# Kernel tuning notes

Measured on AMD Instinct MI355X. Metric: run time of the kernel, lower is better.

The kernel has to match this reference:

```python
import jax, jax.numpy as jnp
import numpy as np

N_NODES = 100000


def _graph_conv(x, W, b, src, dst, inv_sqrt_out, inv_sqrt_in):
    # DGL GraphConv, norm='both':  D_in^{-1/2} A D_out^{-1/2} X W + b
    h = x * inv_sqrt_out[:, None]
    if W.shape[0] > W.shape[1]:
        # in_feats > out_feats: transform first (cheaper aggregation)
        h = h @ W
        m = jax.ops.segment_sum(h[src], dst, num_segments=N_NODES)
    else:
        m = jax.ops.segment_sum(h[src], dst, num_segments=N_NODES)
        m = m @ W
    return m * inv_sqrt_in[:, None] + b


def _degree_norms(src, dst):
    ones = jnp.ones(src.shape[0], dtype=jnp.float32)
    out_deg = jax.ops.segment_sum(ones, src, num_segments=N_NODES)
    in_deg = jax.ops.segment_sum(ones, dst, num_segments=N_NODES)
    # DGL clamps degree to min 1 (allow_zero_in_degree)
    return jnp.clip(out_deg, 1.0) ** -0.5, jnp.clip(in_deg, 1.0) ** -0.5


def setup_inputs() -> dict:
    key = jax.random.key(0)
    ks = jax.random.split(key, 8)
    E = 800000
    in_feats, h1, h2, nc = 128, 256, 128, 40
    return {
        "features": jax.random.normal(ks[0], (N_NODES, in_feats), dtype=jnp.float32),
        "src": jax.random.randint(ks[1], (E,), 0, N_NODES),
        "dst": jax.random.randint(ks[2], (E,), 0, N_NODES),
        "W1": jax.random.normal(ks[3], (in_feats, h1), dtype=jnp.float32) * (2.0 / (in_feats + h1)) ** 0.5,
        "b1": jnp.zeros((h1,), dtype=jnp.float32),
        "W2": jax.random.normal(ks[4], (h1, h2), dtype=jnp.float32) * (2.0 / (h1 + h2)) ** 0.5,
        "b2": jnp.zeros((h2,), dtype=jnp.float32),
        "W3": jax.random.normal(ks[5], (h2, nc), dtype=jnp.float32) * (2.0 / (h2 + nc)) ** 0.5,
        "b3": jnp.zeros((nc,), dtype=jnp.float32),
    }


def reference(features, src, dst, W1, b1, W2, b2, W3, b3):
    inv_out, inv_in = _degree_norms(src, dst)
    h = _graph_conv(features, W1, b1, src, dst, inv_out, inv_in)
    h = jax.nn.relu(h)
    h = _graph_conv(h, W2, b2, src, dst, inv_out, inv_in)
    h = jax.nn.relu(h)
    return _graph_conv(h, W3, b3, src, dst, inv_out, inv_in)
```

## Files before the change

kernel.cpp:

```cpp
#include <hip/hip_runtime.h>

#define N_NODES 100000
#define SCAN_NB 128
#define SCAN_TPB 256
#define NREP 8

typedef _Float16 half_t;
typedef __attribute__((ext_vector_type(8))) _Float16 v8h;
typedef __attribute__((ext_vector_type(4))) _Float16 v4h;
typedef __attribute__((ext_vector_type(4))) float v4f;


__global__ void prep1(const int* __restrict__ src, const int* __restrict__ dst,
                      int* __restrict__ ocntR, int* __restrict__ icntR,
                      int* __restrict__ loc, int E,
                      const float* __restrict__ W1, const float* __restrict__ W2,
                      const float* __restrict__ W3, half_t* __restrict__ Wt1,
                      half_t* __restrict__ Wt2, half_t* __restrict__ Wt3) {
    int t = blockIdx.x * blockDim.x + threadIdx.x;
    if (t < E) {
        int r = (t >> 6) & (NREP - 1);
        loc[t] = atomicAdd(&icntR[r * N_NODES + dst[t]], 1);
        atomicAdd(&ocntR[r * N_NODES + src[t]], 1);
    } else {
        int u = t - E;
        if (u < 32768) {
            int n = u >> 7, k = u & 127;
            Wt1[u] = (half_t)W1[(size_t)k * 256 + n];
        } else if (u < 65536) {
            int w = u - 32768;
            int n = w >> 8, k = w & 255;
            Wt2[w] = (half_t)W2[(size_t)k * 128 + n];
        } else if (u < 70656) {
            int w = u - 65536;
            int n = w >> 7, k = w & 127;
            Wt3[w] = (half_t)W3[(size_t)k * 40 + n];
        }
    }
}


__global__ __launch_bounds__(SCAN_TPB) void scan_reduce(const int* __restrict__ icntR,
                                                        int* __restrict__ blockSum, int n) {
    __shared__ int s[SCAN_TPB];
    int chunk = (n + SCAN_NB - 1) / SCAN_NB;
    int beg = blockIdx.x * chunk;
    int end = min(beg + chunk, n);
    int sum = 0;
    for (int i = beg + threadIdx.x; i < end; i += SCAN_TPB) {
#pragma unroll
        for (int r = 0; r < NREP; ++r) sum += icntR[r * N_NODES + i];
    }
    s[threadIdx.x] = sum;
    __syncthreads();
    for (int off = SCAN_TPB / 2; off > 0; off >>= 1) {
        if (threadIdx.x < off) s[threadIdx.x] += s[threadIdx.x + off];
        __syncthreads();
    }
    if (threadIdx.x == 0) blockSum[blockIdx.x] = s[0];
}

__global__ __launch_bounds__(SCAN_NB) void scan_offsets(int* __restrict__ blockSum,
                                                        int* __restrict__ rowptr_total) {
    __shared__ int s[SCAN_NB];
    int tid = threadIdx.x;
    int v = blockSum[tid];
    s[tid] = v;
    __syncthreads();
    for (int off = 1; off < SCAN_NB; off <<= 1) {
        int t = (tid >= off) ? s[tid - off] : 0;
        __syncthreads();
        s[tid] += t;
        __syncthreads();
    }
    blockSum[tid] = s[tid] - v;
    if (tid == SCAN_NB - 1) rowptr_total[0] = s[tid];
}

__global__ __launch_bounds__(SCAN_TPB) void scan_final(int* __restrict__ icntR,
                                                       const int* __restrict__ ocntR,
                                                       const int* __restrict__ blockSum,
                                                       int* __restrict__ rowptr,
                                                       float* __restrict__ invIn,
                                                       float* __restrict__ invOut, int n) {
    __shared__ int s[SCAN_TPB];
    int chunk = (n + SCAN_NB - 1) / SCAN_NB;
    int beg = blockIdx.x * chunk;
    int end = min(beg + chunk, n);
    int carry = blockSum[blockIdx.x];
    for (int base = beg; base < end; base += SCAN_TPB) {
        int i = base + threadIdx.x;
        int v = 0;
        if (i < end) {
            int run = 0;
#pragma unroll
            for (int r = 0; r < NREP; ++r) {
                int c = icntR[r * N_NODES + i];
                icntR[r * N_NODES + i] = run;
                run += c;
            }
            v = run;
        }
        s[threadIdx.x] = v;
        __syncthreads();
        for (int off = 1; off < SCAN_TPB; off <<= 1) {
            int t = (threadIdx.x >= off) ? s[threadIdx.x - off] : 0;
            __syncthreads();
            s[threadIdx.x] += t;
            __syncthreads();
        }
        int excl = s[threadIdx.x] - v;
        if (i < end) {
            rowptr[i] = carry + excl;
            int o = 0;
#pragma unroll
            for (int r = 0; r < NREP; ++r) o += ocntR[r * N_NODES + i];
            invOut[i] = rsqrtf((float)max(o, 1));
            invIn[i] = rsqrtf((float)max(v, 1));
        }
        int roundSum = s[SCAN_TPB - 1];
        __syncthreads();
        carry += roundSum;
    }
}


__global__ void prep2(const int* __restrict__ src, const int* __restrict__ dst,
                      const int* __restrict__ loc, const int* __restrict__ icntR,
                      const int* __restrict__ rowptr,
                      int* __restrict__ eidx, int E,
                      const float* __restrict__ x, const float* __restrict__ invOut,
                      half_t* __restrict__ xh) {
    int t = blockIdx.x * blockDim.x + threadIdx.x;
    if (t < E) {
        int d = dst[t];
        int r = (t >> 6) & (NREP - 1);
        eidx[rowptr[d] + icntR[r * N_NODES + d] + loc[t]] = src[t];
    } else {
        int u = t - E;
        if (u < N_NODES * 32) {
            int n = u >> 5;
            float4 v = ((const float4*)x)[u];
            float s = invOut[n];
            v4h h;
            h[0] = (half_t)(v.x * s);
            h[1] = (half_t)(v.y * s);
            h[2] = (half_t)(v.z * s);
            h[3] = (half_t)(v.w * s);
            *(v4h*)(xh + (size_t)u * 4) = h;
        }
    }
}


template <int F>
__device__ __forceinline__ void gather_row(const half_t* __restrict__ x,
                                           const int* __restrict__ eidx,
                                           int beg, int end, int c, float* acc) {
    const half_t* __restrict__ xc = x + (size_t)c * 8;
    int n = end - beg;
    int nb = n & ~3;
    int j = 0;
    if (nb) {
        int i0 = eidx[beg + 0], i1 = eidx[beg + 1], i2 = eidx[beg + 2], i3 = eidx[beg + 3];
        do {
            v8h v0 = *(const v8h*)(xc + (size_t)i0 * F);
            v8h v1 = *(const v8h*)(xc + (size_t)i1 * F);
            v8h v2 = *(const v8h*)(xc + (size_t)i2 * F);
            v8h v3 = *(const v8h*)(xc + (size_t)i3 * F);
            j += 4;
            if (j < nb) {
                i0 = eidx[beg + j + 0];
                i1 = eidx[beg + j + 1];
                i2 = eidx[beg + j + 2];
                i3 = eidx[beg + j + 3];
            }
#pragma unroll
            for (int q = 0; q < 8; ++q)
                acc[q] += ((float)v0[q] + (float)v1[q]) + ((float)v2[q] + (float)v3[q]);
        } while (j < nb);
    }
    for (; j < n; ++j) {
        int s = eidx[beg + j];
        v8h val = *(const v8h*)(xc + (size_t)s * F);
#pragma unroll
        for (int q = 0; q < 8; ++q) acc[q] += (float)val[q];
    }
}


__global__ __launch_bounds__(256, 8) void gather1(
    const half_t* __restrict__ xh, const int* __restrict__ rowptr,
    const int* __restrict__ eidx, half_t* __restrict__ A1) {
    int t = blockIdx.x * 256 + threadIdx.x;
    int n = t >> 4, c = t & 15;
    if (n >= N_NODES) return;
    float acc[8] = {};
    gather_row<128>(xh, eidx, rowptr[n], rowptr[n + 1], c, acc);
    v8h o;
#pragma unroll
    for (int q = 0; q < 8; ++q) o[q] = (half_t)acc[q];
    *(v8h*)(A1 + (size_t)n * 128 + c * 8) = o;
}

__global__ __launch_bounds__(256, 8) void gather2(
    const half_t* __restrict__ t2, const int* __restrict__ rowptr,
    const int* __restrict__ eidx, const float* __restrict__ invIn,
    const float* __restrict__ invOut, const float* __restrict__ b2,
    half_t* __restrict__ A2) {
    int t = blockIdx.x * 256 + threadIdx.x;
    int n = t >> 4, c = t & 15;
    if (n >= N_NODES) return;
    float acc[8] = {};
    gather_row<128>(t2, eidx, rowptr[n], rowptr[n + 1], c, acc);
    float ii = invIn[n], io = invOut[n];
    float4 blo = ((const float4*)b2)[c * 2];
    float4 bhi = ((const float4*)b2)[c * 2 + 1];
    float bb[8] = {blo.x, blo.y, blo.z, blo.w, bhi.x, bhi.y, bhi.z, bhi.w};
    v8h o;
#pragma unroll
    for (int q = 0; q < 8; ++q)
        o[q] = (half_t)fmaxf((acc[q] * ii + bb[q]) * io, 0.f);
    *(v8h*)(A2 + (size_t)n * 128 + c * 8) = o;
}


__global__ __launch_bounds__(512) void mlp12(
    const half_t* __restrict__ A1, const half_t* __restrict__ Wt1,
    const half_t* __restrict__ Wt2,
    const float* __restrict__ invIn, const float* __restrict__ invOut,
    const float* __restrict__ b1, half_t* __restrict__ t2) {
    constexpr int K1 = 128, K2 = 256, N2 = 128;
    constexpr int LDA = K1 + 8;
    constexpr int LDH = K2 + 8;
    __shared__ half_t As[64][LDA];
    __shared__ half_t h1S[64][LDH];
    __shared__ float iiS[64], ioS[64];
    const int tid = threadIdx.x;
    const int wave = tid >> 6, lane = tid & 63;
    const int quad = lane >> 4, l16 = lane & 15;
    const int m0 = blockIdx.x * 64;
    const int n0 = wave * 32;

    v8h b[2][4];
    float bv[2];
#pragma unroll
    for (int j = 0; j < 2; ++j) {
        int gn = n0 + j * 16 + l16;
        bv[j] = b1[gn];
#pragma unroll
        for (int kc = 0; kc < 4; ++kc)
            b[j][kc] = *(const v8h*)(Wt1 + (size_t)gn * K1 + kc * 32 + quad * 8);
    }
    if (tid < 64) {
        int gm = m0 + tid;
        bool ok = gm < N_NODES;
        iiS[tid] = ok ? invIn[gm] : 0.f;
        ioS[tid] = ok ? invOut[gm] : 0.f;
    }

#pragma unroll
    for (int p = 0; p < 2; ++p) {
        int task = tid + p * 512;
        int r = task >> 4, c = task & 15;
        int gm = m0 + r;
        v8h v = (gm < N_NODES) ? *(const v8h*)(A1 + (size_t)gm * K1 + c * 8)
                               : (v8h)(half_t)0;
        *(v8h*)&As[r][c * 8] = v;
    }
    __syncthreads();

    for (int mt = 0; mt < 4; ++mt) {
        v8h a[4];
#pragma unroll
        for (int kc = 0; kc < 4; ++kc)
            a[kc] = *(const v8h*)&As[mt * 16 + l16][kc * 32 + quad * 8];
        v4f acc[2] = {};
#pragma unroll
        for (int kc = 0; kc < 4; ++kc)
#pragma unroll
            for (int j = 0; j < 2; ++j)
                acc[j] = __builtin_amdgcn_mfma_f32_16x16x32_f16(a[kc], b[j][kc], acc[j], 0, 0, 0);
#pragma unroll
        for (int j = 0; j < 2; ++j) {
            int cn = n0 + j * 16 + l16;
#pragma unroll
            for (int r = 0; r < 4; ++r) {
                int lr = mt * 16 + quad * 4 + r;
                float z = (acc[j][r] * iiS[lr] + bv[j]) * ioS[lr];
                h1S[lr][cn] = (half_t)fmaxf(z, 0.f);
            }
        }
    }

    v8h b2[8];
    const int n02 = wave * 16;
    {
        int gn = n02 + l16;
#pragma unroll
        for (int kc = 0; kc < 8; ++kc)
            b2[kc] = *(const v8h*)(Wt2 + (size_t)gn * K2 + kc * 32 + quad * 8);
    }
    __syncthreads();

    for (int mt = 0; mt < 4; ++mt) {
        v8h a2[8];
#pragma unroll
        for (int kc = 0; kc < 8; ++kc)
            a2[kc] = *(const v8h*)&h1S[mt * 16 + l16][kc * 32 + quad * 8];
        v4f acc2 = {};
#pragma unroll
        for (int kc = 0; kc < 8; ++kc)
            acc2 = __builtin_amdgcn_mfma_f32_16x16x32_f16(a2[kc], b2[kc], acc2, 0, 0, 0);
        int gn = n02 + l16;
#pragma unroll
        for (int r = 0; r < 4; ++r) {
            int gm = m0 + mt * 16 + quad * 4 + r;
            if (gm < N_NODES) t2[(size_t)gm * N2 + gn] = (half_t)acc2[r];
        }
    }
}


__global__ __launch_bounds__(256) void mlp3(
    const half_t* __restrict__ A2, const half_t* __restrict__ Wt3,
    half_t* __restrict__ t3) {
    constexpr int K = 128, N = 40, LDA = K + 8;
    __shared__ half_t As[64][LDA];
    const int tid = threadIdx.x;
    const int wave = tid >> 6, lane = tid & 63;
    const int quad = lane >> 4, l16 = lane & 15;
    const int m0 = blockIdx.x * 64;

    v8h b[3][4];
#pragma unroll
    for (int j = 0; j < 3; ++j) {
        int gn = j * 16 + l16;
#pragma unroll
        for (int kc = 0; kc < 4; ++kc)
            b[j][kc] = (gn < N) ? *(const v8h*)(Wt3 + (size_t)gn * K + kc * 32 + quad * 8)
                                : (v8h)(half_t)0;
    }

#pragma unroll
    for (int p = 0; p < 4; ++p) {
        int task = tid + p * 256;
        int r = task >> 4, c = task & 15;
        int gm = m0 + r;
        v8h v = (gm < N_NODES) ? *(const v8h*)(A2 + (size_t)gm * K + c * 8)
                               : (v8h)(half_t)0;
        *(v8h*)&As[r][c * 8] = v;
    }
    __syncthreads();

    {
        int mt = wave;
        v8h a[4];
#pragma unroll
        for (int kc = 0; kc < 4; ++kc)
            a[kc] = *(const v8h*)&As[mt * 16 + l16][kc * 32 + quad * 8];
        v4f acc[3] = {};
#pragma unroll
        for (int kc = 0; kc < 4; ++kc)
#pragma unroll
            for (int j = 0; j < 3; ++j)
                acc[j] = __builtin_amdgcn_mfma_f32_16x16x32_f16(a[kc], b[j][kc], acc[j], 0, 0, 0);
#pragma unroll
        for (int j = 0; j < 3; ++j) {
            int gn = j * 16 + l16;
            if (gn >= N) continue;
#pragma unroll
            for (int r = 0; r < 4; ++r) {
                int gm = m0 + mt * 16 + quad * 4 + r;
                if (gm < N_NODES) t3[(size_t)gm * N + gn] = (half_t)acc[j][r];
            }
        }
    }
}


__global__ __launch_bounds__(256, 8) void gather_final(
    const half_t* __restrict__ x,
    const int* __restrict__ rowptr, const int* __restrict__ eidx,
    float* __restrict__ out, const float* __restrict__ invIn,
    const float* __restrict__ bias) {
    constexpr int F = 40, V = 5;
    int t = blockIdx.x * blockDim.x + threadIdx.x;
    int n = t / V;
    int v = t - n * V;
    if (n >= N_NODES) return;
    float acc[8] = {};
    gather_row<F>(x, eidx, rowptr[n], rowptr[n + 1], v, acc);
    float ii = invIn[n];
    float* o = out + (size_t)n * F + v * 8;
#pragma unroll
    for (int q = 0; q < 8; ++q) o[q] = acc[q] * ii + bias[v * 8 + q];
}


extern "C" void kernel_launch(void* const* d_in, const int* in_sizes, int n_in,
                              void* d_out, int out_size, void* d_ws, size_t ws_size,
                              hipStream_t stream) {
    const float* x  = (const float*)d_in[0];
    const int* src  = (const int*)d_in[1];
    const int* dst  = (const int*)d_in[2];
    const float* W1 = (const float*)d_in[3];
    const float* b1 = (const float*)d_in[4];
    const float* W2 = (const float*)d_in[5];
    const float* b2 = (const float*)d_in[6];
    const float* W3 = (const float*)d_in[7];
    const float* b3 = (const float*)d_in[8];
    float* out = (float*)d_out;
    const int E = in_sizes[1];

    char* ws = (char*)d_ws;
    float* inv_out = (float*)ws;
    float* inv_in  = (float*)(ws + 400000);
    int* rowptr    = (int*)(ws + 800000);
    int* eidx      = (int*)(ws + 1600256);
    int* blockSum  = (int*)(ws + 4800256);
    half_t* Wt1    = (half_t*)(ws + 4800768);
    half_t* Wt2    = (half_t*)(ws + 4866304);
    half_t* Wt3    = (half_t*)(ws + 4931840);
    half_t* bufA   = (half_t*)(ws + 5000192);
    half_t* bufB   = (half_t*)(ws + 30600192);
    int* loc   = (int*)bufB;
    int* icntR = (int*)((char*)bufB + (((size_t)E * 4 + 255) & ~(size_t)255));
    int* ocntR = icntR + NREP * N_NODES;

    hipMemsetAsync(icntR, 0, (size_t)NREP * N_NODES * 4 * 2, stream);
    prep1<<<(E + 70656 + 255) / 256, 256, 0, stream>>>(src, dst, ocntR, icntR, loc, E,
                                                       W1, W2, W3, Wt1, Wt2, Wt3);
    scan_reduce<<<SCAN_NB, SCAN_TPB, 0, stream>>>(icntR, blockSum, N_NODES);
    scan_offsets<<<1, SCAN_NB, 0, stream>>>(blockSum, rowptr + N_NODES);
    scan_final<<<SCAN_NB, SCAN_TPB, 0, stream>>>(icntR, ocntR, blockSum, rowptr,
                                                 inv_in, inv_out, N_NODES);
    prep2<<<(E + N_NODES * 32 + 255) / 256, 256, 0, stream>>>(src, dst, loc, icntR, rowptr,
                                                              eidx, E, x, inv_out, bufA);

    const int NBG = (N_NODES * 16 + 255) / 256;
    const int NB  = (N_NODES + 63) / 64;

    gather1<<<NBG, 256, 0, stream>>>(bufA, rowptr, eidx, bufB);
    mlp12<<<NB, 512, 0, stream>>>(bufB, Wt1, Wt2, inv_in, inv_out, b1, bufA);
    gather2<<<NBG, 256, 0, stream>>>(bufA, rowptr, eidx, inv_in, inv_out, b2, bufB);
    mlp3<<<NB, 256, 0, stream>>>(bufB, Wt3, bufA);
    gather_final<<<(N_NODES * 5 + 255) / 256, 256, 0, stream>>>(
        bufA, rowptr, eidx, out, inv_in, b3);
}
```

Before: 338.8 us.

## Replace global atomic degree counting with LDS-privatized sliced histograms

Degree counting now runs in shared-memory histograms: each block covers one 12500-node bin range and one of 32 edge slices, and writes 16-bit partial counts instead of doing global atomics across 8 replicas. The scan and scatter kernels are reworked to read these per-slice partials, which give each edge its CSR position, and the memset is dropped. The aim is to remove contended global atomics. The cost is that every block reads its whole edge slice for a single bin group, so edge data is read 8 times for each of src and dst, and the scans must sum 32 slices per node.

```diff
diff --git a/kernel.cpp b/kernel.cpp
--- a/kernel.cpp
+++ b/kernel.cpp
@@ -3,7 +3,9 @@
 #define N_NODES 100000
 #define SCAN_NB 128
 #define SCAN_TPB 256
-#define NREP 8
+#define GCOUNT 8
+#define BINS 12500
+#define NSLICE 32
 
 typedef _Float16 half_t;
 typedef __attribute__((ext_vector_type(8))) _Float16 v8h;
@@ -11,19 +13,44 @@
 typedef __attribute__((ext_vector_type(4))) float v4f;
 
 
-__global__ void prep1(const int* __restrict__ src, const int* __restrict__ dst,
-                      int* __restrict__ ocntR, int* __restrict__ icntR,
-                      int* __restrict__ loc, int E,
-                      const float* __restrict__ W1, const float* __restrict__ W2,
-                      const float* __restrict__ W3, half_t* __restrict__ Wt1,
-                      half_t* __restrict__ Wt2, half_t* __restrict__ Wt3) {
-    int t = blockIdx.x * blockDim.x + threadIdx.x;
-    if (t < E) {
-        int r = (t >> 6) & (NREP - 1);
-        loc[t] = atomicAdd(&icntR[r * N_NODES + dst[t]], 1);
-        atomicAdd(&ocntR[r * N_NODES + src[t]], 1);
+__global__ __launch_bounds__(512) void hist_all(
+    const int* __restrict__ src, const int* __restrict__ dst,
+    int* __restrict__ loc, unsigned short* __restrict__ partialI,
+    unsigned short* __restrict__ partialO, int E,
+    const float* __restrict__ W1, const float* __restrict__ W2,
+    const float* __restrict__ W3, half_t* __restrict__ Wt1,
+    half_t* __restrict__ Wt2, half_t* __restrict__ Wt3) {
+    __shared__ int hist[BINS];
+    const int bid = blockIdx.x;
+    const int tid = threadIdx.x;
+    if (bid < 2 * GCOUNT * NSLICE) {
+        const bool isDst = bid < GCOUNT * NSLICE;
+        const int b2 = isDst ? bid : bid - GCOUNT * NSLICE;
+        const int g = b2 >> 5, s = b2 & (NSLICE - 1);
+        const int gbase = g * BINS;
+        for (int b = tid; b < BINS; b += 512) hist[b] = 0;
+        __syncthreads();
+        const int chunk = (E + NSLICE - 1) / NSLICE;
+        const int e0 = s * chunk;
+        const int e1 = min(e0 + chunk, E);
+        if (isDst) {
+            for (int e = e0 + tid; e < e1; e += 512) {
+                int d = dst[e];
+                unsigned lb = (unsigned)(d - gbase);
+                if (lb < (unsigned)BINS) loc[e] = atomicAdd(&hist[lb], 1);
+            }
+        } else {
+            for (int e = e0 + tid; e < e1; e += 512) {
+                int d = src[e];
+                unsigned lb = (unsigned)(d - gbase);
+                if (lb < (unsigned)BINS) atomicAdd(&hist[lb], 1);
+            }
+        }
+        __syncthreads();
+        unsigned short* p = (isDst ? partialI : partialO) + (size_t)b2 * BINS;
+        for (int b = tid; b < BINS; b += 512) p[b] = (unsigned short)hist[b];
     } else {
-        int u = t - E;
+        int u = (bid - 2 * GCOUNT * NSLICE) * 512 + tid;
         if (u < 32768) {
             int n = u >> 7, k = u & 127;
             Wt1[u] = (half_t)W1[(size_t)k * 256 + n];
@@ -40,16 +67,18 @@
 }
 
 
-__global__ __launch_bounds__(SCAN_TPB) void scan_reduce(const int* __restrict__ icntR,
-                                                        int* __restrict__ blockSum, int n) {
+__global__ __launch_bounds__(SCAN_TPB) void scan_reduce(
+    const unsigned short* __restrict__ partialI, int* __restrict__ blockSum, int n) {
     __shared__ int s[SCAN_TPB];
     int chunk = (n + SCAN_NB - 1) / SCAN_NB;
     int beg = blockIdx.x * chunk;
     int end = min(beg + chunk, n);
     int sum = 0;
     for (int i = beg + threadIdx.x; i < end; i += SCAN_TPB) {
-#pragma unroll
-        for (int r = 0; r < NREP; ++r) sum += icntR[r * N_NODES + i];
+        int g = i / BINS, lb = i - g * BINS;
+        const unsigned short* p = partialI + (size_t)g * NSLICE * BINS + lb;
+#pragma unroll
+        for (int sl = 0; sl < NSLICE; ++sl) sum += p[(size_t)sl * BINS];
     }
     s[threadIdx.x] = sum;
     __syncthreads();
@@ -77,12 +106,10 @@
     if (tid == SCAN_NB - 1) rowptr_total[0] = s[tid];
 }
 
-__global__ __launch_bounds__(SCAN_TPB) void scan_final(int* __restrict__ icntR,
-                                                       const int* __restrict__ ocntR,
-                                                       const int* __restrict__ blockSum,
-                                                       int* __restrict__ rowptr,
-                                                       float* __restrict__ invIn,
-                                                       float* __restrict__ invOut, int n) {
+__global__ __launch_bounds__(SCAN_TPB) void scan_final(
+    unsigned short* __restrict__ partialI, const unsigned short* __restrict__ partialO,
+    const int* __restrict__ blockSum, int* __restrict__ rowptr,
+    float* __restrict__ invIn, float* __restrict__ invOut, int n) {
     __shared__ int s[SCAN_TPB];
     int chunk = (n + SCAN_NB - 1) / SCAN_NB;
     int beg = blockIdx.x * chunk;
@@ -90,16 +117,21 @@
     int carry = blockSum[blockIdx.x];
     for (int base = beg; base < end; base += SCAN_TPB) {
         int i = base + threadIdx.x;
-        int v = 0;
+        int v = 0, o = 0;
         if (i < end) {
+            int g = i / BINS, lb = i - g * BINS;
+            unsigned short* p = partialI + (size_t)g * NSLICE * BINS + lb;
             int run = 0;
 #pragma unroll
-            for (int r = 0; r < NREP; ++r) {
-                int c = icntR[r * N_NODES + i];
-                icntR[r * N_NODES + i] = run;
+            for (int sl = 0; sl < NSLICE; ++sl) {
+                int c = p[(size_t)sl * BINS];
+                p[(size_t)sl * BINS] = (unsigned short)run;
                 run += c;
             }
             v = run;
+            const unsigned short* q = partialO + (size_t)g * NSLICE * BINS + lb;
+#pragma unroll
+            for (int sl = 0; sl < NSLICE; ++sl) o += q[(size_t)sl * BINS];
         }
         s[threadIdx.x] = v;
         __syncthreads();
@@ -112,9 +144,6 @@
         int excl = s[threadIdx.x] - v;
         if (i < end) {
             rowptr[i] = carry + excl;
-            int o = 0;
-#pragma unroll
-            for (int r = 0; r < NREP; ++r) o += ocntR[r * N_NODES + i];
             invOut[i] = rsqrtf((float)max(o, 1));
             invIn[i] = rsqrtf((float)max(v, 1));
         }
@@ -126,7 +155,8 @@
 
 
 __global__ void prep2(const int* __restrict__ src, const int* __restrict__ dst,
-                      const int* __restrict__ loc, const int* __restrict__ icntR,
+                      const int* __restrict__ loc,
+                      const unsigned short* __restrict__ partialI,
                       const int* __restrict__ rowptr,
                       int* __restrict__ eidx, int E,
                       const float* __restrict__ x, const float* __restrict__ invOut,
@@ -134,8 +164,11 @@
     int t = blockIdx.x * blockDim.x + threadIdx.x;
     if (t < E) {
         int d = dst[t];
-        int r = (t >> 6) & (NREP - 1);
-        eidx[rowptr[d] + icntR[r * N_NODES + d] + loc[t]] = src[t];
+        int chunk = (E + NSLICE - 1) / NSLICE;
+        int s = t / chunk;
+        int g = d / BINS, lb = d - g * BINS;
+        int pre = partialI[(size_t)(g * NSLICE + s) * BINS + lb];
+        eidx[rowptr[d] + pre + loc[t]] = src[t];
     } else {
         int u = t - E;
         if (u < N_NODES * 32) {
@@ -424,19 +457,20 @@
     half_t* Wt3    = (half_t*)(ws + 4931840);
     half_t* bufA   = (half_t*)(ws + 5000192);
     half_t* bufB   = (half_t*)(ws + 30600192);
-    int* loc   = (int*)bufB;
-    int* icntR = (int*)((char*)bufB + (((size_t)E * 4 + 255) & ~(size_t)255));
-    int* ocntR = icntR + NREP * N_NODES;
-
-    hipMemsetAsync(icntR, 0, (size_t)NREP * N_NODES * 4 * 2, stream);
-    prep1<<<(E + 70656 + 255) / 256, 256, 0, stream>>>(src, dst, ocntR, icntR, loc, E,
-                                                       W1, W2, W3, Wt1, Wt2, Wt3);
-    scan_reduce<<<SCAN_NB, SCAN_TPB, 0, stream>>>(icntR, blockSum, N_NODES);
+    int* loc = (int*)bufB;
+    unsigned short* partialI = (unsigned short*)((char*)bufB + 3200000);
+    unsigned short* partialO = partialI + (size_t)GCOUNT * NSLICE * BINS;
+
+    const int NBH = 2 * GCOUNT * NSLICE + (70656 + 511) / 512;
+    hist_all<<<NBH, 512, 0, stream>>>(src, dst, loc, partialI, partialO, E,
+                                      W1, W2, W3, Wt1, Wt2, Wt3);
+    scan_reduce<<<SCAN_NB, SCAN_TPB, 0, stream>>>(partialI, blockSum, N_NODES);
     scan_offsets<<<1, SCAN_NB, 0, stream>>>(blockSum, rowptr + N_NODES);
-    scan_final<<<SCAN_NB, SCAN_TPB, 0, stream>>>(icntR, ocntR, blockSum, rowptr,
+    scan_final<<<SCAN_NB, SCAN_TPB, 0, stream>>>(partialI, partialO, blockSum, rowptr,
                                                  inv_in, inv_out, N_NODES);
-    prep2<<<(E + N_NODES * 32 + 255) / 256, 256, 0, stream>>>(src, dst, loc, icntR, rowptr,
-                                                              eidx, E, x, inv_out, bufA);
+    prep2<<<(E + N_NODES * 32 + 255) / 256, 256, 0, stream>>>(src, dst, loc, partialI,
+                                                              rowptr, eidx, E,
+                                                              x, inv_out, bufA);
 
     const int NBG = (N_NODES * 16 + 255) / 256;
     const int NB  = (N_NODES + 63) / 64;
```

Result: faster. 298.8 us (-11.8%).
